# Performance work log

Measured on AMD Instinct MI355X. Metric: run time of the kernel, lower is better.

The kernel has to match this reference:

```python
import jax, jax.numpy as jnp
import numpy as np

T, IO, H, M = 8192, 32, 256, 4  # timesteps, io_width, hidden_width, max ponder steps
EPS = 0.01  # ACT halting epsilon


def setup_inputs() -> dict:
    key = jax.random.key(0)
    ks = jax.random.split(key, 8)
    sc = 0.05
    return {
        "x": jax.random.normal(ks[0], (T, IO), jnp.float32),
        "h0": jnp.zeros((H,), jnp.float32),                       # act1_h initial state
        "Wp": jax.random.normal(ks[1], (H, IO), jnp.float32) * sc,  # input_processing Linear
        "bp": jnp.zeros((H,), jnp.float32),
        "Wx": jax.random.normal(ks[2], (H, H + 1), jnp.float32) * sc,  # ACT cell input weights (+1 first-step flag)
        "Ws": jax.random.normal(ks[3], (H, H), jnp.float32) * sc,      # ACT cell recurrent weights
        "b": jnp.zeros((H,), jnp.float32),
        "wh": jax.random.normal(ks[4], (H,), jnp.float32) * sc,        # halting unit
        "bh": jnp.float32(1.0),
        "Wo": jax.random.normal(ks[5], (IO, H), jnp.float32) * sc,     # ACT output projection
        "bo": jnp.zeros((IO,), jnp.float32),
    }


def reference(x, h0, Wp, bp, Wx, Ws, b, wh, bh, Wo, bo):
    # Faithful translation: per-timestep loop (lax.scan) over the sequence; each step
    # runs input_processing then an ACT (Graves) ponder loop with max M=4 steps.
    # io_noise is identity in eval mode. attention_beam_width=1 => line == current point.
    T_ = x.shape[0]

    def step(carry, x_t):
        h, pc = carry
        lin1 = Wp @ x_t + bp  # [H]
        s = h
        cum = jnp.float32(0.0)
        acc_s = jnp.zeros_like(h)
        acc_y = jnp.zeros_like(bo)
        n_up = jnp.float32(0.0)
        rem = jnp.float32(0.0)
        still = jnp.bool_(True)
        for n in range(M):  # fixed small ponder loop, masked ACT halting
            flag = jnp.full((1,), 1.0 if n == 0 else 0.0, lin1.dtype)
            inp = jnp.concatenate([lin1, flag])  # [H+1]
            s = jnp.tanh(Wx @ inp + Ws @ s + b)
            p = jax.nn.sigmoid(wh @ s + bh)
            halt = (cum + p > 1.0 - EPS) | (n == M - 1)
            w = jnp.where(still, jnp.where(halt, 1.0 - cum, p), 0.0)
            acc_s = acc_s + w * s
            acc_y = acc_y + w * (Wo @ s + bo)
            rem = rem + jnp.where(still & halt, 1.0 - cum, 0.0)
            n_up = n_up + jnp.where(still, 1.0, 0.0)
            cum = cum + w
            still = still & jnp.logical_not(halt)
        ponder = n_up + rem  # N(t) + R(t)
        pc = (pc + ponder) / jnp.float32(T_)  # matches the in-loop division in the original forward
        return (acc_s, pc), acc_y

    (_, pc), ys = jax.lax.scan(step, (h0, jnp.float32(0.0)), x)
    return ys, pc
```

## Files before the change

kernel.cpp:

```cpp
#include <hip/hip_runtime.h>


#define T_  8192
#define IO_ 32
#define H_  256

typedef __attribute__((ext_vector_type(2))) float v2f;

template<int CTRL>
__device__ __forceinline__ float dpp_addf(float x) {
    int xi = __builtin_bit_cast(int, x);
    int d = __builtin_amdgcn_update_dpp(xi, xi, CTRL, 0xF, 0xF, false);
    return x + __builtin_bit_cast(float, d);
}

__global__ void k_prep(const float* __restrict__ Wx,
                       const float* __restrict__ Wp,
                       const float* __restrict__ bp,
                       const float* __restrict__ b,
                       float* __restrict__ WxpT, float* __restrict__ cvec) {
    int h = blockIdx.x;
    int t = threadIdx.x;
    __shared__ float wxrow[H_];
    for (int j = t; j < H_; j += 64) wxrow[j] = Wx[h * (H_ + 1) + j];
    __syncthreads();
    if (t < IO_) {
        float acc = 0.0f;
        for (int j = 0; j < H_; ++j) acc += wxrow[j] * Wp[j * IO_ + t];
        WxpT[t * H_ + h] = acc;
    } else if (t == IO_) {
        float acc = b[h];
        for (int j = 0; j < H_; ++j) acc += wxrow[j] * bp[j];
        cvec[h] = acc;
    }
}

__global__ void k_u(const float* __restrict__ x,
                    const float* __restrict__ WxpT,
                    const float* __restrict__ cvec,
                    float* __restrict__ U) {
    int t0 = blockIdx.x * 8;
    int tid = threadIdx.x;
    __shared__ float xsf[8 * IO_];
    xsf[tid] = x[(size_t)t0 * IO_ + tid];
    __syncthreads();
    int h = tid;
    float base = cvec[h];
    for (int tt = 0; tt < 8; ++tt) {
        float acc = base;
        #pragma unroll
        for (int io = 0; io < IO_; ++io)
            acc += WxpT[io * H_ + h] * xsf[tt * IO_ + io];
        U[(size_t)(t0 + tt) * H_ + h] = acc;
    }
}

__global__ __launch_bounds__(512, 2) void act_chain(
    const float* __restrict__ Ws,
    const float* __restrict__ Wx,
    const float* __restrict__ wh,
    const float* __restrict__ bh1,
    const float* __restrict__ h0,
    float* __restrict__ UAcc,
    float* __restrict__ cumArr,
    float* __restrict__ pc_out)
{
    __shared__ __align__(16) float sbuf[2][4 * 68];
    __shared__ __align__(16) float plds[2][8];

    const int tid = threadIdx.x;
    const int w   = tid >> 6;
    const int l   = tid & 63;
    const int rg  = l >> 2;
    const int c   = l & 3;
    const int rowbase = w * 32 + rg * 2;
    const int schunk  = rowbase >> 6;
    const int soff    = rowbase & 63;

    v2f wt[2][32];
    #pragma unroll
    for (int r = 0; r < 2; ++r) {
        const float4* src = (const float4*)(Ws + (size_t)(rowbase + r) * H_ + c * 64);
        #pragma unroll
        for (int q = 0; q < 16; ++q) {
            float4 f = src[q];
            wt[r][2 * q]     = (v2f){f.x, f.y};
            wt[r][2 * q + 1] = (v2f){f.z, f.w};
        }
    }

    v2f wl2, whv2;
    wl2.x  = Wx[(size_t)rowbase * (H_ + 1) + H_];
    wl2.y  = Wx[(size_t)(rowbase + 1) * (H_ + 1) + H_];
    whv2.x = wh[rowbase];
    whv2.y = wh[rowbase + 1];
    const float bhf = bh1[0];
    const float thresh = 1.0f - 0.01f;
    const float L2E  = 1.4426950408889634f;
    const float L2E2 = 2.8853900817779268f;

    if (tid < H_) sbuf[0][(tid >> 6) * 68 + (tid & 63)] = h0[tid];
    __syncthreads();

    int cur = 0, pp = 0;
    float pc = 0.0f;

    #pragma unroll 1
    for (int tg = 0; tg < T_ / 4; ++tg) {
        v2f un[4];
        #pragma unroll
        for (int k = 0; k < 4; ++k)
            un[k] = *(const v2f*)(UAcc + (size_t)(tg * 4 + k) * H_ + rowbase);

        v2f   av[4];
        float cu4[4];

        #pragma unroll
        for (int k = 0; k < 4; ++k) {
            const v2f uu1 = un[k];
            const v2f uu0 = uu1 + wl2;

            v2f accs = {0.f, 0.f};
            float cum = 0.0f, nup = 0.0f, remt = 0.0f;
            float sn0, sn1;

            #pragma unroll 1
            for (int n = 0; n < 4; ++n) {
                v2f acc0 = {0.f, 0.f}, acc1 = {0.f, 0.f};
                const float4* sp = (const float4*)(&sbuf[cur][c * 68]);
                #pragma unroll
                for (int q = 0; q < 16; ++q) {
                    float4 f = sp[q];
                    v2f sa = (v2f){f.x, f.y};
                    v2f sb = (v2f){f.z, f.w};
                    acc0 = acc0 + wt[0][2 * q] * sa;
                    acc0 = acc0 + wt[0][2 * q + 1] * sb;
                    acc1 = acc1 + wt[1][2 * q] * sa;
                    acc1 = acc1 + wt[1][2 * q + 1] * sb;
                }
                float y0 = acc0.x + acc0.y;
                float y1 = acc1.x + acc1.y;
                y0 = dpp_addf<0xB1>(y0); y0 = dpp_addf<0x4E>(y0);
                y1 = dpp_addf<0xB1>(y1); y1 = dpp_addf<0x4E>(y1);

                v2f uu = (n == 0) ? uu0 : uu1;
                float yy0 = y0 + uu.x;
                float yy1 = y1 + uu.y;
                float e0 = __builtin_amdgcn_exp2f(yy0 * L2E2);
                float e1 = __builtin_amdgcn_exp2f(yy1 * L2E2);
                sn0 = __builtin_fmaf(-2.0f, __builtin_amdgcn_rcpf(e0 + 1.0f), 1.0f);
                sn1 = __builtin_fmaf(-2.0f, __builtin_amdgcn_rcpf(e1 + 1.0f), 1.0f);

                int nxt = cur ^ 1;
                if (c == 0)
                    *(v2f*)(&sbuf[nxt][schunk * 68 + soff]) = (v2f){sn0, sn1};

                float part = __builtin_fmaf(whv2.x, sn0, whv2.y * sn1);
                part = dpp_addf<0x124>(part);
                part = dpp_addf<0x128>(part);
                part = dpp_addf<0x142>(part);
                part = dpp_addf<0x143>(part);
                if (l == 63) plds[pp][w] = part;
                __syncthreads();

                float4 pa = *(const float4*)(&plds[pp][0]);
                float4 pb = *(const float4*)(&plds[pp][4]);
                float dot = ((pa.x + pa.y) + (pa.z + pa.w)) +
                            ((pb.x + pb.y) + (pb.z + pb.w));
                pp ^= 1;
                float p = __builtin_amdgcn_rcpf(
                    1.0f + __builtin_amdgcn_exp2f(-(dot + bhf) * L2E));
                bool halt = (cum + p > thresh) || (n == 3);
                float hw = 1.0f - cum;
                float wn = halt ? hw : p;
                accs = accs + wn * (v2f){sn0, sn1};
                nup += 1.0f;
                cum += wn;
                if (halt) { remt = hw; break; }
                cur = nxt;
            }

            pc = (pc + nup + remt) * (1.0f / (float)T_);

            int hb = cur ^ 1;
            av[k]  = accs;
            cu4[k] = cum;
            if (c == 0)
                *(v2f*)(&sbuf[hb][schunk * 68 + soff]) = accs;
            cur = hb;
            __syncthreads();
        }

        if (c == 0) {
            #pragma unroll
            for (int k = 0; k < 4; ++k)
                *(v2f*)(UAcc + (size_t)(tg * 4 + k) * H_ + rowbase) = av[k];
        }
        if (tid == 0) {
            #pragma unroll
            for (int k = 0; k < 4; ++k) cumArr[tg * 4 + k] = cu4[k];
        }
    }
    if (tid == 0) pc_out[0] = pc;
}

__global__ void k_out(const float* __restrict__ AccS,
                      const float* __restrict__ Wo,
                      const float* __restrict__ bo,
                      const float* __restrict__ cumArr,
                      float* __restrict__ ys) {
    int t0 = blockIdx.x * 8;
    int tid = threadIdx.x;
    __shared__ float wo[IO_ * 257];
    __shared__ float as[8 * 260];
    for (int i = tid; i < IO_ * H_; i += 256) {
        int o = i / H_, h = i % H_;
        wo[o * 257 + h] = Wo[i];
    }
    for (int i = tid; i < 8 * H_; i += 256) {
        int tt = i / H_, h = i % H_;
        as[tt * 260 + h] = AccS[(size_t)t0 * H_ + i];
    }
    __syncthreads();
    int tt = tid >> 5, o = tid & 31;
    float acc = cumArr[t0 + tt] * bo[o];
    #pragma unroll 4
    for (int h = 0; h < H_; ++h) acc += wo[o * 257 + h] * as[tt * 260 + h];
    ys[(size_t)(t0 + tt) * IO_ + o] = acc;
}

extern "C" void kernel_launch(void* const* d_in, const int* in_sizes, int n_in,
                              void* d_out, int out_size, void* d_ws, size_t ws_size,
                              hipStream_t stream) {
    const float* x  = (const float*)d_in[0];
    const float* h0 = (const float*)d_in[1];
    const float* Wp = (const float*)d_in[2];
    const float* bp = (const float*)d_in[3];
    const float* Wx = (const float*)d_in[4];
    const float* Ws = (const float*)d_in[5];
    const float* b  = (const float*)d_in[6];
    const float* wh = (const float*)d_in[7];
    const float* bh = (const float*)d_in[8];
    const float* Wo = (const float*)d_in[9];
    const float* bo = (const float*)d_in[10];
    float* out = (float*)d_out;

    char* ws = (char*)d_ws;
    float* WxpT = (float*)ws;
    float* cvec = (float*)(ws + 32768);
    float* cumA = (float*)(ws + 33792);
    float* UAcc = (float*)(ws + 66560);

    k_prep<<<H_, 64, 0, stream>>>(Wx, Wp, bp, b, WxpT, cvec);
    k_u<<<T_ / 8, 256, 0, stream>>>(x, WxpT, cvec, UAcc);
    act_chain<<<1, 512, 0, stream>>>(Ws, Wx, wh, bh, h0, UAcc, cumA,
                                     out + (size_t)T_ * IO_);
    k_out<<<T_ / 8, 256, 0, stream>>>(UAcc, Wo, bo, cumA, out);
}
```

Baseline: 12.10 ms.

## Carry recurrent matvec linearly across steps to drop one barrier per timestep

```diff
diff --git a/kernel.cpp b/kernel.cpp
--- a/kernel.cpp
+++ b/kernel.cpp
@@ -12,6 +12,40 @@
     int xi = __builtin_bit_cast(int, x);
     int d = __builtin_amdgcn_update_dpp(xi, xi, CTRL, 0xF, 0xF, false);
     return x + __builtin_bit_cast(float, d);
+}
+template<int CTRL>
+__device__ __forceinline__ float dpp_get(float x) {
+    int xi = __builtin_bit_cast(int, x);
+    int d = __builtin_amdgcn_update_dpp(xi, xi, CTRL, 0xF, 0xF, false);
+    return __builtin_bit_cast(float, d);
+}
+__device__ __forceinline__ float swz_xor4(float x) {
+    return __builtin_bit_cast(float,
+        __builtin_amdgcn_ds_swizzle(__builtin_bit_cast(int, x), 0x101F));
+}
+__device__ __forceinline__ void bar_lds() {
+    asm volatile("s_waitcnt lgkmcnt(0)\n\ts_barrier" ::: "memory");
+    __builtin_amdgcn_sched_barrier(0);
+}
+
+__device__ __forceinline__ float mv_reduce(const v2f (&wt)[8][8], const v2f (&sc)[8]) {
+    float v[8];
+    #pragma unroll
+    for (int k = 0; k < 8; ++k) {
+        v2f a = wt[k][0] * sc[0];
+        #pragma unroll
+        for (int q = 1; q < 8; ++q) a += wt[k][q] * sc[q];
+        v[k] = a.x + a.y;
+    }
+    v[0] += dpp_get<0x128>(v[4]);
+    v[1] += dpp_get<0x128>(v[5]);
+    v[2] += dpp_get<0x128>(v[6]);
+    v[3] += dpp_get<0x128>(v[7]);
+    v[0] += dpp_get<0x4E>(v[2]);
+    v[1] += dpp_get<0x4E>(v[3]);
+    v[0] += swz_xor4(v[1]);
+    v[0] += dpp_get<0xB1>(v[0]);
+    return v[0];
 }
 
 __global__ void k_prep(const float* __restrict__ Wx,
@@ -46,12 +80,13 @@
     __syncthreads();
     int h = tid;
     float base = cvec[h];
+    const float L2E2 = 2.8853900817779268f;
     for (int tt = 0; tt < 8; ++tt) {
         float acc = base;
         #pragma unroll
         for (int io = 0; io < IO_; ++io)
             acc += WxpT[io * H_ + h] * xsf[tt * IO_ + io];
-        U[(size_t)(t0 + tt) * H_ + h] = acc;
+        U[(size_t)(t0 + tt) * H_ + h] = acc * L2E2;
     }
 }
 
@@ -65,141 +100,106 @@
     float* __restrict__ cumArr,
     float* __restrict__ pc_out)
 {
-    __shared__ __align__(16) float sbuf[2][4 * 68];
+    __shared__ __align__(16) float sbuf[2][320];
     __shared__ __align__(16) float plds[2][8];
 
     const int tid = threadIdx.x;
     const int w   = tid >> 6;
     const int l   = tid & 63;
-    const int rg  = l >> 2;
-    const int c   = l & 3;
-    const int rowbase = w * 32 + rg * 2;
-    const int schunk  = rowbase >> 6;
-    const int soff    = rowbase & 63;
-
-    v2f wt[2][32];
-    #pragma unroll
-    for (int r = 0; r < 2; ++r) {
-        const float4* src = (const float4*)(Ws + (size_t)(rowbase + r) * H_ + c * 64);
-        #pragma unroll
-        for (int q = 0; q < 16; ++q) {
-            float4 f = src[q];
-            wt[r][2 * q]     = (v2f){f.x, f.y};
-            wt[r][2 * q + 1] = (v2f){f.z, f.w};
-        }
-    }
-
-    v2f wl2, whv2;
-    wl2.x  = Wx[(size_t)rowbase * (H_ + 1) + H_];
-    wl2.y  = Wx[(size_t)(rowbase + 1) * (H_ + 1) + H_];
-    whv2.x = wh[rowbase];
-    whv2.y = wh[rowbase + 1];
-    const float bhf = bh1[0];
-    const float thresh = 1.0f - 0.01f;
+    const int cb  = l & 15;
+    const int g   = ((l & 8) >> 1) | (l & 2) | ((l & 4) >> 2);
+    const int rbase = w * 32 + (l >> 4) * 8;
+    const int r_own = rbase + g;
+    const int swidx = (r_own >> 4) * 20 + (r_own & 15);
+
     const float L2E  = 1.4426950408889634f;
     const float L2E2 = 2.8853900817779268f;
 
-    if (tid < H_) sbuf[0][(tid >> 6) * 68 + (tid & 63)] = h0[tid];
-    __syncthreads();
-
-    int cur = 0, pp = 0;
+    v2f wt[8][8];
+    #pragma unroll
+    for (int k = 0; k < 8; ++k) {
+        const float4* s4 = (const float4*)(Ws + (size_t)(rbase + (k ^ g)) * H_ + cb * 16);
+        #pragma unroll
+        for (int q = 0; q < 4; ++q) {
+            float4 f = s4[q];
+            wt[k][2 * q]     = (v2f){f.x * L2E2, f.y * L2E2};
+            wt[k][2 * q + 1] = (v2f){f.z * L2E2, f.w * L2E2};
+        }
+    }
+
+    const float wlf = Wx[(size_t)r_own * (H_ + 1) + H_] * L2E2;
+    const float whp = wh[r_own] * (-L2E);
+    const float bhp = -bh1[0] * L2E;
+    const float thresh = 1.0f - 0.01f;
+
+    float zh;
+    {
+        v2f sc[8];
+        const float4* hp = (const float4*)(h0 + cb * 16);
+        #pragma unroll
+        for (int q = 0; q < 4; ++q) {
+            float4 f = hp[q];
+            sc[2 * q]     = (v2f){f.x, f.y};
+            sc[2 * q + 1] = (v2f){f.z, f.w};
+        }
+        zh = mv_reduce(wt, sc);
+    }
+
+    int wb = 0, pp = 0;
     float pc = 0.0f;
+    float un_cur = UAcc[r_own];
 
     #pragma unroll 1
-    for (int tg = 0; tg < T_ / 4; ++tg) {
-        v2f un[4];
-        #pragma unroll
-        for (int k = 0; k < 4; ++k)
-            un[k] = *(const v2f*)(UAcc + (size_t)(tg * 4 + k) * H_ + rowbase);
-
-        v2f   av[4];
-        float cu4[4];
-
-        #pragma unroll
-        for (int k = 0; k < 4; ++k) {
-            const v2f uu1 = un[k];
-            const v2f uu0 = uu1 + wl2;
-
-            v2f accs = {0.f, 0.f};
-            float cum = 0.0f, nup = 0.0f, remt = 0.0f;
-            float sn0, sn1;
-
-            #pragma unroll 1
-            for (int n = 0; n < 4; ++n) {
-                v2f acc0 = {0.f, 0.f}, acc1 = {0.f, 0.f};
-                const float4* sp = (const float4*)(&sbuf[cur][c * 68]);
-                #pragma unroll
-                for (int q = 0; q < 16; ++q) {
-                    float4 f = sp[q];
-                    v2f sa = (v2f){f.x, f.y};
-                    v2f sb = (v2f){f.z, f.w};
-                    acc0 = acc0 + wt[0][2 * q] * sa;
-                    acc0 = acc0 + wt[0][2 * q + 1] * sb;
-                    acc1 = acc1 + wt[1][2 * q] * sa;
-                    acc1 = acc1 + wt[1][2 * q + 1] * sb;
-                }
-                float y0 = acc0.x + acc0.y;
-                float y1 = acc1.x + acc1.y;
-                y0 = dpp_addf<0xB1>(y0); y0 = dpp_addf<0x4E>(y0);
-                y1 = dpp_addf<0xB1>(y1); y1 = dpp_addf<0x4E>(y1);
-
-                v2f uu = (n == 0) ? uu0 : uu1;
-                float yy0 = y0 + uu.x;
-                float yy1 = y1 + uu.y;
-                float e0 = __builtin_amdgcn_exp2f(yy0 * L2E2);
-                float e1 = __builtin_amdgcn_exp2f(yy1 * L2E2);
-                sn0 = __builtin_fmaf(-2.0f, __builtin_amdgcn_rcpf(e0 + 1.0f), 1.0f);
-                sn1 = __builtin_fmaf(-2.0f, __builtin_amdgcn_rcpf(e1 + 1.0f), 1.0f);
-
-                int nxt = cur ^ 1;
-                if (c == 0)
-                    *(v2f*)(&sbuf[nxt][schunk * 68 + soff]) = (v2f){sn0, sn1};
-
-                float part = __builtin_fmaf(whv2.x, sn0, whv2.y * sn1);
-                part = dpp_addf<0x124>(part);
-                part = dpp_addf<0x128>(part);
-                part = dpp_addf<0x142>(part);
-                part = dpp_addf<0x143>(part);
-                if (l == 63) plds[pp][w] = part;
-                __syncthreads();
-
-                float4 pa = *(const float4*)(&plds[pp][0]);
-                float4 pb = *(const float4*)(&plds[pp][4]);
-                float dot = ((pa.x + pa.y) + (pa.z + pa.w)) +
-                            ((pb.x + pb.y) + (pb.z + pb.w));
-                pp ^= 1;
-                float p = __builtin_amdgcn_rcpf(
-                    1.0f + __builtin_amdgcn_exp2f(-(dot + bhf) * L2E));
-                bool halt = (cum + p > thresh) || (n == 3);
-                float hw = 1.0f - cum;
-                float wn = halt ? hw : p;
-                accs = accs + wn * (v2f){sn0, sn1};
-                nup += 1.0f;
-                cum += wn;
-                if (halt) { remt = hw; break; }
-                cur = nxt;
-            }
-
-            pc = (pc + nup + remt) * (1.0f / (float)T_);
-
-            int hb = cur ^ 1;
-            av[k]  = accs;
-            cu4[k] = cum;
-            if (c == 0)
-                *(v2f*)(&sbuf[hb][schunk * 68 + soff]) = accs;
-            cur = hb;
-            __syncthreads();
+    for (int t = 0; t < T_; ++t) {
+        const int tn = (t + 1 < T_) ? t + 1 : t;
+        const float un_nxt = UAcc[(size_t)tn * H_ + r_own];
+
+        float accs = 0.0f, zacc = 0.0f;
+        float cum = 0.0f, nup = 0.0f, remt = 0.0f;
+        float zin = zh;
+        float uadd = un_cur + wlf;
+
+        #pragma unroll 1
+        for (int n = 0; n < 4; ++n) {
+            float e = __builtin_amdgcn_exp2f(zin + uadd);
+            float s = __builtin_fmaf(-2.0f, __builtin_amdgcn_rcpf(e + 1.0f), 1.0f);
+            sbuf[wb][swidx] = s;
+            float part = whp * s;
+            part = dpp_addf<0x4E>(part);
+            part = dpp_addf<0x124>(part);
+            part = dpp_addf<0x128>(part);
+            part = dpp_addf<0x142>(part);
+            part = dpp_addf<0x143>(part);
+            if (l == 63) plds[pp][w] = part;
+            bar_lds();
+            const float4* sp = (const float4*)(&sbuf[wb][cb * 20]);
+            const float4* pr = (const float4*)(&plds[pp][0]);
+            wb ^= 1; pp ^= 1;
+            float4 qa = pr[0], qb = pr[1];
+            float4 f0 = sp[0], f1 = sp[1], f2 = sp[2], f3 = sp[3];
+            v2f sc[8] = {{f0.x, f0.y}, {f0.z, f0.w}, {f1.x, f1.y}, {f1.z, f1.w},
+                         {f2.x, f2.y}, {f2.z, f2.w}, {f3.x, f3.y}, {f3.z, f3.w}};
+            float z = mv_reduce(wt, sc);
+            float dot = ((qa.x + qa.y) + (qa.z + qa.w)) +
+                        ((qb.x + qb.y) + (qb.z + qb.w));
+            float p = __builtin_amdgcn_rcpf(1.0f + __builtin_amdgcn_exp2f(dot + bhp));
+            bool halt = (cum + p > thresh) || (n == 3);
+            float hw = 1.0f - cum;
+            float wn = halt ? hw : p;
+            accs = __builtin_fmaf(wn, s, accs);
+            zacc = __builtin_fmaf(wn, z, zacc);
+            nup += 1.0f;
+            cum += wn;
+            if (halt) { remt = hw; break; }
+            zin = z;
+            uadd = un_cur;
         }
 
-        if (c == 0) {
-            #pragma unroll
-            for (int k = 0; k < 4; ++k)
-                *(v2f*)(UAcc + (size_t)(tg * 4 + k) * H_ + rowbase) = av[k];
-        }
-        if (tid == 0) {
-            #pragma unroll
-            for (int k = 0; k < 4; ++k) cumArr[tg * 4 + k] = cu4[k];
-        }
+        pc = (pc + nup + remt) * (1.0f / (float)T_);
+        zh = zacc;
+        if ((l & 1) == 0) UAcc[(size_t)t * H_ + r_own] = accs;
+        if (tid == 0) cumArr[t] = cum;
+        un_cur = un_nxt;
     }
     if (tid == 0) pc_out[0] = pc;
 }
```

New measurement: 13.16 ms. 1.09x slower.
